# Kernel tuning notes

Measured on AMD Instinct MI355X. Metric: run time of the kernel, lower is better.

The kernel has to match this reference:

```python
import jax, jax.numpy as jnp
import numpy as np

B, K, N = 32768, 8, 64
TN = 3 * N


def _P():
    # 9x9 vec-transpose permutation (matches the hand-built P in the torch module)
    P = np.zeros((9, 9), dtype=np.float32)
    rows = [0, 1, 2, 3, 4, 5, 6, 7, 8]
    cols = [0, 3, 6, 1, 4, 7, 2, 5, 8]
    P[rows, cols] = 1.0
    return jnp.asarray(P)


def _precompute(b, w, lam):
    # b: (K,3,N), w: (1,N,1), lam: scalar
    wsum = jnp.sum(w)
    b_w = (b @ w)[..., 0] / wsum                       # (K,3)
    sw = jnp.sqrt(w).reshape(1, 1, N)                  # (1,1,N)
    bar_b = sw * (b - b_w[:, :, None])                 # (K,3,N)
    bar_B = bar_b.transpose(0, 2, 1).reshape(K, TN).T  # (3N,K)
    bar_H = 2.0 * (bar_B.T @ bar_B + lam * jnp.eye(K, dtype=b.dtype))
    Hinv = jnp.linalg.inv(bar_H)
    Htemp = Hinv @ jnp.ones((K, 1), dtype=b.dtype)     # (K,1)
    s = jnp.sum(Htemp)
    G = Hinv - (Htemp @ Htemp.T) / s                   # (K,K)
    g = Htemp / s                                      # (K,1)
    M = jnp.concatenate([
        2.0 * bar_B @ (G @ bar_B.T) - jnp.eye(TN, dtype=b.dtype),  # (3N,3N)
        2.0 * jnp.sqrt(lam) * (G @ bar_B.T),                        # (K,3N)
    ], axis=0)                                         # (3N+K,3N)
    h = jnp.concatenate([bar_B @ g, jnp.sqrt(lam) * g], axis=0)  # (3N+K,1)
    return bar_B, G, g, M, h, b_w, wsum


def setup_inputs() -> dict:
    key = jax.random.key(0)
    k1, k2 = jax.random.split(key)
    y = jax.random.normal(k1, (B, 3, N), dtype=jnp.float32)
    b = jax.random.normal(k2, (K, 3, N), dtype=jnp.float32)
    w = jnp.ones((1, N, 1), dtype=jnp.float32)
    lam = jnp.ones((1,), dtype=jnp.float32)
    return {"y": y, "b": b, "w": w, "lam": lam}


def reference(y, b, w, lam):
    lam = jnp.squeeze(lam)
    Pm = _P()
    bar_B, G, g, M, h, b_w, wsum = _precompute(b, w, lam)

    # weighted centroid + centered/weighted keypoints
    y_w = (y @ w) / wsum                               # (B,3,1)
    sw = jnp.sqrt(w).reshape(1, 1, N)
    bar_y = sw * (y - y_w)                             # (B,3,N)

    # Batched Q build. kron(Y^T, I3) contraction done implicitly:
    # (M @ kron(Y^T,I3))[a, 3m+j] = sum_n M[a,3n+j] * Y[m,n]
    M_r = M.reshape(TN + K, N, 3)                      # (A,N,3)
    E = jnp.einsum('anj,bmn->bamj', M_r, bar_y).reshape(B, TN + K, 9) @ Pm  # tempE: (B,A,9)
    q_top = jnp.einsum('a,bae->be', h[:, 0], E)        # Q[0,1:]: (B,9)
    Q00 = jnp.sum(h * h)
    Q_low = jnp.einsum('bae,baf->bef', E, E)           # Q[1:,1:]: (B,9,9)

    Q = jnp.zeros((B, 10, 10), dtype=y.dtype)
    Q = Q.at[:, 0, 0].set(Q00)
    Q = Q.at[:, 0, 1:].set(q_top)
    Q = Q.at[:, 1:, 0].set(q_top)
    Q = Q.at[:, 1:, 1:].set(Q_low)

    # Tight SDP relaxation solution: X* = v v^T with v the eigenvector of Q
    # at the smallest eigenvalue; the original then takes top eigvec of X,
    # which recovers the same v.
    ev, evec = jnp.linalg.eigh(Q)
    vec = evec[:, :, 0]                                # smallest-eigenvalue eigvec, (B,10)
    vec = vec / vec[:, :1]
    R = vec[:, 1:].reshape(B, 3, 3).transpose(0, 2, 1)  # (B,3,3)

    # shape coefficients: c = 2 * G bar_B^T kron(I_N, R^T) vec(bar_y^T) + g
    A = G @ bar_B.T                                    # (K,3N)
    Bv = jnp.einsum('bji,bjn->bni', R, bar_y).reshape(B, TN, 1)
    c = 2.0 * (A @ Bv) + g                             # (B,K,1)

    # translation
    t = y_w - R @ (b_w.T @ c)                          # (B,3,1)
    return R, t, c
```

## Files before the change

kernel.cpp:

```cpp
#include <hip/hip_runtime.h>
#include <math.h>

static constexpr int Bn = 32768;

__host__ __device__ constexpr int tidx(int i, int j) { return i*10 - i*(i+1)/2 + j; }
__host__ __device__ constexpr int lidx(int i, int j) { return i*(i+1)/2 + j; }

__global__ __launch_bounds__(256, 2) void k_main(const float* __restrict__ y,
                                                 const float* __restrict__ bb,
                                                 const float* __restrict__ w,
                                                 const float* __restrict__ lam,
                                                 float* __restrict__ out)
{
  __shared__ float s_w[64], s_sw[64], s_barb[64][24];
  __shared__ float s_BtB[64];
  __shared__ float s_M[8][16];
  __shared__ float s_u[8], s_red[64];
  __shared__ float s_wsum, s_q00;
  __shared__ float s_cb[4*520];
  __shared__ float s_G[64], s_g8[8], s_bw[24];
  __shared__ float s_Q[55][66];

  const int t   = threadIdx.x;
  const bool act = (t < 64);
  const int i8 = (t & 63) >> 3, j8 = t & 7;
  const float lv = lam[0];

  if (act) {
    s_w[t]  = w[t];
    s_sw[t] = sqrtf(fmaxf(w[t], 0.0f));
  }
  __syncthreads();
  if (t == 0) { float a = 0; for (int n = 0; n < 64; n++) a += s_w[n]; s_wsum = a; }
  __syncthreads();
  const float wsum = s_wsum;
  if (t < 24) {
    float a = 0;
    for (int n = 0; n < 64; n++) a += bb[t*64 + n] * s_w[n];
    s_bw[t] = a / wsum;
  }
  __syncthreads();
  if (act)
    for (int km = 0; km < 24; ++km)
      s_barb[t][km] = s_sw[t] * (bb[km*64 + t] - s_bw[km]);
  __syncthreads();
  if (act) {
    float a = 0;
    for (int n = 0; n < 64; n++)
      for (int j = 0; j < 3; j++)
        a += s_barb[n][i8*3 + j] * s_barb[n][j8*3 + j];
    s_BtB[t] = a;
  }
  __syncthreads();
  if (act) {
    s_M[i8][j8]     = 2.0f * (s_BtB[t] + ((i8 == j8) ? lv : 0.0f));
    s_M[i8][8 + j8] = (i8 == j8) ? 1.0f : 0.0f;
  }
#pragma unroll
  for (int k = 0; k < 8; k++) {
    __syncthreads();
    float fk = 0.0f, piv = 1.0f;
    if (act) { fk = s_M[i8][k]; piv = 1.0f / s_M[k][k]; }
    __syncthreads();
    if (act && i8 == k) { s_M[k][j8] *= piv; s_M[k][8 + j8] *= piv; }
    __syncthreads();
    if (act && i8 != k) {
      s_M[i8][j8]     -= fk * s_M[k][j8];
      s_M[i8][8 + j8] -= fk * s_M[k][8 + j8];
    }
  }
  __syncthreads();
  if (t < 8) {
    float a = 0;
#pragma unroll
    for (int j = 0; j < 8; j++) a += s_M[t][8 + j];
    s_u[t] = a;
  }
  __syncthreads();
  if (t == 0) {
    float s = 0;
#pragma unroll
    for (int j = 0; j < 8; j++) s += s_u[j];
    s_red[0] = s;
  }
  __syncthreads();
  {
    const float s = s_red[0];
    if (t < 8) s_g8[t] = s_u[t] / s;
    if (act) s_G[t] = s_M[i8][8 + j8] - s_u[i8] * s_u[j8] / s;
  }
  __syncthreads();
  if (act) s_red[t] = s_g8[i8] * (s_BtB[t] + ((i8 == j8) ? lv : 0.0f)) * s_g8[j8];
  __syncthreads();
  if (t == 0) {
    float a = 0;
    for (int n = 0; n < 64; n++) a += s_red[n];
    s_q00 = a;
  }
  if (act) {
    float* p = s_cb + (t >> 4)*520 + (t & 15)*32;
    p[0] = s_w[t]; p[1] = 0; p[2] = 0; p[3] = 0;
#pragma unroll
    for (int km = 0; km < 24; km++)
      p[4 + km] = s_sw[t] * s_barb[t][km];
#pragma unroll
    for (int i = 28; i < 32; i++) p[i] = 0;
  }
  __syncthreads();
  const float q00v = s_q00;

  const int lb  = t >> 2;
  const int sub = t & 3;
  const int b   = blockIdx.x * 64 + lb;
  const float* yb = y + (size_t)b * 192;
  float F[24][3];
  float gw[6];
  float ywa[3] = {0, 0, 0};
#pragma unroll
  for (int i = 0; i < 24; i++) { F[i][0] = 0; F[i][1] = 0; F[i][2] = 0; }
#pragma unroll
  for (int i = 0; i < 6; i++) gw[i] = 0;

  const float* plane = s_cb + sub*520;
#pragma unroll
  for (int i4 = 0; i4 < 4; i4++) {
    const int n4 = sub*4 + i4;
    float4 v0 = reinterpret_cast<const float4*>(yb)[n4];
    float4 v1 = reinterpret_cast<const float4*>(yb + 64)[n4];
    float4 v2 = reinterpret_cast<const float4*>(yb + 128)[n4];
    float a0[4] = {v0.x, v0.y, v0.z, v0.w};
    float a1[4] = {v1.x, v1.y, v1.z, v1.w};
    float a2[4] = {v2.x, v2.y, v2.z, v2.w};
#pragma unroll
    for (int l = 0; l < 4; l++) {
      const int ni = 4*i4 + l;
      const float4* row = reinterpret_cast<const float4*>(plane + ni*32);
      float4 c0 = row[0];
      float4 ch[6];
#pragma unroll
      for (int cc = 0; cc < 6; cc++) ch[cc] = row[1 + cc];
      const float cb[24] = {ch[0].x, ch[0].y, ch[0].z, ch[0].w,
                            ch[1].x, ch[1].y, ch[1].z, ch[1].w,
                            ch[2].x, ch[2].y, ch[2].z, ch[2].w,
                            ch[3].x, ch[3].y, ch[3].z, ch[3].w,
                            ch[4].x, ch[4].y, ch[4].z, ch[4].w,
                            ch[5].x, ch[5].y, ch[5].z, ch[5].w};
      float ym0 = a0[l], ym1 = a1[l], ym2 = a2[l];
      float wn  = c0.x;
      float wy0 = wn*ym0, wy1 = wn*ym1, wy2 = wn*ym2;
      ywa[0] += wy0; ywa[1] += wy1; ywa[2] += wy2;
      gw[0] += wy0*ym0; gw[1] += wy0*ym1; gw[2] += wy0*ym2;
      gw[3] += wy1*ym1; gw[4] += wy1*ym2; gw[5] += wy2*ym2;
#pragma unroll
      for (int km = 0; km < 24; km++) {
        F[km][0] += cb[km]*ym0; F[km][1] += cb[km]*ym1; F[km][2] += cb[km]*ym2;
      }
    }
  }
#pragma unroll
  for (int km = 0; km < 24; km++)
#pragma unroll
    for (int m = 0; m < 3; m++) {
      float v = F[km][m];
      v += __shfl_xor(v, 1);
      v += __shfl_xor(v, 2);
      F[km][m] = v;
    }
#pragma unroll
  for (int i = 0; i < 6; i++) { float v = gw[i]; v += __shfl_xor(v, 1); v += __shfl_xor(v, 2); gw[i] = v; }
#pragma unroll
  for (int i = 0; i < 3; i++) { float v = ywa[i]; v += __shfl_xor(v, 1); v += __shfl_xor(v, 2); ywa[i] = v; }

  const float iws = 1.0f / wsum;
  float yw[3] = {ywa[0]*iws, ywa[1]*iws, ywa[2]*iws};
  float Gram[6];
  Gram[0] = gw[0] - ywa[0]*ywa[0]*iws;
  Gram[1] = gw[1] - ywa[0]*ywa[1]*iws;
  Gram[2] = gw[2] - ywa[0]*ywa[2]*iws;
  Gram[3] = gw[3] - ywa[1]*ywa[1]*iws;
  Gram[4] = gw[4] - ywa[1]*ywa[2]*iws;
  Gram[5] = gw[5] - ywa[2]*ywa[2]*iws;

  if (sub == 0) s_Q[0][lb] = q00v;
#pragma unroll
  for (int e = 0; e < 9; e++) {
    const int j = e / 3, m = e % 3;
    float a = 0;
#pragma unroll
    for (int k = 0; k < 8; k++) a += s_g8[k] * F[k*3 + j][m];
    if ((e & 3) == sub) s_Q[tidx(0, 1 + e)][lb] = -a;
  }
  float F6[6][3];
#pragma unroll
  for (int kk = 0; kk < 6; kk++)
#pragma unroll
    for (int m = 0; m < 3; m++) {
      float x01 = (sub & 1) ? F[6 + kk][m]  : F[kk][m];
      float x23 = (sub & 1) ? F[18 + kk][m] : F[12 + kk][m];
      F6[kk][m] = (sub & 2) ? x23 : x01;
    }
  float FGr[2][9];
#pragma unroll
  for (int kk = 0; kk < 2; kk++) {
    float gcol[8];
#pragma unroll
    for (int k = 0; k < 8; k++) {
      float g01 = (sub & 1) ? s_G[k*8 + 2 + kk] : s_G[k*8 + 0 + kk];
      float g23 = (sub & 1) ? s_G[k*8 + 6 + kk] : s_G[k*8 + 4 + kk];
      gcol[k] = (sub & 2) ? g23 : g01;
    }
#pragma unroll
    for (int e = 0; e < 9; e++) {
      const int j = e / 3, m = e % 3;
      float a = 0;
#pragma unroll
      for (int k = 0; k < 8; k++) a += gcol[k] * F[k*3 + j][m];
      FGr[kk][e] = a;
    }
  }
#pragma unroll
  for (int e = 0; e < 9; e++)
#pragma unroll
    for (int f = e; f < 9; f++) {
      const int j = e/3, m = e%3, j2 = f/3, m2 = f%3;
      float p = FGr[0][e] * F6[j2][m2] + FGr[1][e] * F6[3 + j2][m2];
      p += __shfl_xor(p, 1);
      p += __shfl_xor(p, 2);
      if ((tidx(1 + e, 1 + f) & 3) == sub) {
        const float gterm = (j == j2) ? Gram[(m <= m2) ? (m*3 - m*(m+1)/2 + m2) : (m2*3 - m2*(m2+1)/2 + m)] : 0.0f;
        s_Q[tidx(1 + e, 1 + f)][lb] = -2.0f*p + gterm;
      }
    }
  __syncthreads();

  float Mm[55];
#pragma unroll
  for (int i = 0; i < 10; i++)
#pragma unroll
    for (int j = 0; j <= i; j++)
      Mm[lidx(i,j)] = s_Q[tidx(j,i)][lb];

  float ad[10], b2[9];
#pragma unroll
  for (int j = 0; j < 8; j++) {
    float s2 = 0;
#pragma unroll
    for (int i = j + 1; i < 10; i++) s2 += Mm[lidx(i,j)] * Mm[lidx(i,j)];
    const float x0 = Mm[lidx(j+1,j)];
    const float anorm = __builtin_amdgcn_sqrtf(s2);
    const float alpha = (x0 > 0.0f) ? -anorm : anorm;
    const float uu = s2 - alpha * x0;
    const float beta = (uu > 1e-35f) ? __builtin_amdgcn_rcpf(uu) : 0.0f;
    float u[10], p[10];
    u[j+1] = x0 - alpha;
#pragma unroll
    for (int i = j + 2; i < 10; i++) u[i] = Mm[lidx(i,j)];
#pragma unroll
    for (int i = j + 1; i < 10; i++) {
      float acc = 0;
#pragma unroll
      for (int k = j + 1; k < 10; k++) acc += Mm[(i >= k) ? lidx(i,k) : lidx(k,i)] * u[k];
      p[i] = beta * acc;
    }
    float K = 0;
#pragma unroll
    for (int i = j + 1; i < 10; i++) K += u[i] * p[i];
    K *= 0.5f * beta;
#pragma unroll
    for (int i = j + 1; i < 10; i++) p[i] -= K * u[i];
#pragma unroll
    for (int i = j + 1; i < 10; i++)
#pragma unroll
      for (int k = j + 1; k <= i; k++)
        Mm[lidx(i,k)] -= u[i]*p[k] + p[i]*u[k];
    ad[j] = Mm[lidx(j,j)];
    b2[j] = s2;
  }
  ad[8] = Mm[lidx(8,8)];
  ad[9] = Mm[lidx(9,9)];
  b2[8] = Mm[lidx(9,8)] * Mm[lidx(9,8)];

  float b2max = b2[0];
#pragma unroll
  for (int i = 1; i < 9; i++) b2max = fmaxf(b2max, b2[i]);
  const float pm = 1e-20f * b2max + 1e-30f;

  float lo = 0.0f, hi = s_Q[0][lb];
#pragma unroll
  for (int j = 1; j < 10; j++) hi = fminf(hi, s_Q[tidx(j,j)][lb]);

  const int base = (t & 63) & ~3;
  const float subf = (sub == 0) ? 2.0f : (float)sub;
  for (int round = 0; round < 11; ++round) {
    const float quart = 0.25f * (hi - lo);
    const float mid = lo + quart * subf;
    int neg = 0;
    float d = ad[0] - mid;
    neg += (d < 0.0f) ? 1 : 0;
#pragma unroll
    for (int i = 1; i < 10; i++) {
      d = (fabsf(d) < pm) ? -pm : d;
      d = ad[i] - mid - b2[i-1] * __builtin_amdgcn_rcpf(d);
      neg += (d < 0.0f) ? 1 : 0;
    }
    const int n1 = __shfl(neg, base | 1);
    const int n2 = __shfl(neg, base | 2);
    const int n3 = __shfl(neg, base | 3);
    const float m1 = lo + quart, m2v = lo + 2.0f*quart, m3 = lo + 3.0f*quart;
    const float nlo = (n3 == 0) ? m3 : (n2 == 0) ? m2v : (n1 == 0) ? m1 : lo;
    const float nhi = (n1 > 0) ? m1 : (n2 > 0) ? m2v : (n3 > 0) ? m3 : hi;
    lo = nlo; hi = nhi;
  }

  float M[55], id[10];
#pragma unroll
  for (int i = 0; i < 10; i++)
#pragma unroll
    for (int j = 0; j <= i; j++)
      M[lidx(i,j)] = s_Q[tidx(j,i)][lb];
  float tr = 0.0f;
#pragma unroll
  for (int i = 0; i < 10; i++) tr += M[lidx(i,i)];
  const float delta = 1e-5f * fabsf(tr) + 1e-30f;
  const float sigma = lo - delta;
#pragma unroll
  for (int i = 0; i < 10; i++) M[lidx(i,i)] -= sigma;

#pragma unroll
  for (int j = 0; j < 10; j++) {
    float d = M[lidx(j,j)];
#pragma unroll
    for (int t2 = 0; t2 < j; t2++) d -= M[lidx(j,t2)] * M[lidx(j,t2)];
    d = fmaxf(d, 1e-30f);
    float is = __builtin_amdgcn_rsqf(d);
    id[j] = is;
#pragma unroll
    for (int i = j + 1; i < 10; i++) {
      float a = M[lidx(i,j)];
#pragma unroll
      for (int t2 = 0; t2 < j; t2++) a -= M[lidx(i,t2)] * M[lidx(j,t2)];
      M[lidx(i,j)] = a * is;
    }
  }

  float x[10];
#pragma unroll
  for (int i = 0; i < 10; i++) x[i] = 1.0f;
#pragma unroll
  for (int it = 0; it < 3; ++it) {
#pragma unroll
    for (int i = 0; i < 10; i++) {
      float a = x[i];
#pragma unroll
      for (int j = 0; j < i; j++) a -= M[lidx(i,j)] * x[j];
      x[i] = a * id[i];
    }
#pragma unroll
    for (int i = 9; i >= 0; i--) {
      float a = x[i];
#pragma unroll
      for (int j = i + 1; j < 10; j++) a -= M[lidx(j,i)] * x[j];
      x[i] = a * id[i];
    }
    float s2 = 0;
#pragma unroll
    for (int i = 0; i < 10; i++) s2 += x[i]*x[i];
    float sc = __builtin_amdgcn_rsqf(s2 + 1e-38f);
#pragma unroll
    for (int i = 0; i < 10; i++) x[i] *= sc;
  }

  const float inv0 = __builtin_amdgcn_rcpf(x[0]);
  float R[3][3];
#pragma unroll
  for (int r = 0; r < 3; r++)
#pragma unroll
    for (int cc = 0; cc < 3; cc++)
      R[r][cc] = x[1 + 3*cc + r] * inv0;

  float cv[2];
#pragma unroll
  for (int kk = 0; kk < 2; kk++) {
    const int k = sub*2 + kk;
    float a = 0;
#pragma unroll
    for (int e = 0; e < 9; e++) a += x[1 + e] * FGr[kk][e];
    cv[kk] = 2.0f * inv0 * a + s_g8[k];
    out[(size_t)12*Bn + (size_t)b*8 + k] = cv[kk];
  }
  float um0 = s_bw[(sub*2)*3 + 0]*cv[0] + s_bw[(sub*2 + 1)*3 + 0]*cv[1];
  float um1 = s_bw[(sub*2)*3 + 1]*cv[0] + s_bw[(sub*2 + 1)*3 + 1]*cv[1];
  float um2 = s_bw[(sub*2)*3 + 2]*cv[0] + s_bw[(sub*2 + 1)*3 + 2]*cv[1];
  um0 += __shfl_xor(um0, 1); um0 += __shfl_xor(um0, 2);
  um1 += __shfl_xor(um1, 1); um1 += __shfl_xor(um1, 2);
  um2 += __shfl_xor(um2, 1); um2 += __shfl_xor(um2, 2);

#pragma unroll
  for (int r = 0; r < 3; r++)
#pragma unroll
    for (int cc = 0; cc < 3; cc++)
      if (((r*3 + cc) & 3) == sub)
        out[(size_t)b*9 + r*3 + cc] = R[r][cc];
  if (sub == 0) {
#pragma unroll
    for (int r = 0; r < 3; r++)
      out[(size_t)9*Bn + (size_t)b*3 + r] = yw[r] - (R[r][0]*um0 + R[r][1]*um1 + R[r][2]*um2);
  }
}

extern "C" void kernel_launch(void* const* d_in, const int* in_sizes, int n_in,
                              void* d_out, int out_size, void* d_ws, size_t ws_size,
                              hipStream_t stream) {
  const float* y   = (const float*)d_in[0];
  const float* bb  = (const float*)d_in[1];
  const float* w   = (const float*)d_in[2];
  const float* lam = (const float*)d_in[3];
  float* out = (float*)d_out;
  (void)d_ws; (void)ws_size;
  k_main<<<Bn/64, 256, 0, stream>>>(y, bb, w, lam, out);
}
```

Measured before the change: 38.50 us.

## Keep Q in registers and do inverse iteration on the tridiagonal form

Drops the shared-memory Q staging buffer and its barrier: each lane now builds the full symmetric 10x10 Q in registers from the shuffle-reduced values. Inverse iteration now runs on the Householder tridiagonal matrix with an LDL factorization instead of a dense Cholesky of the shifted Q. The eigenvector is then mapped back by applying the stored Householder reflectors in reverse. This removes the dense Cholesky, dense triangular solves and repeated LDS reads, but it raises register pressure because all 55 entries of Q stay live, and it uses an unpivoted tridiagonal LDL.

```diff
diff --git a/kernel.cpp b/kernel.cpp
--- a/kernel.cpp
+++ b/kernel.cpp
@@ -3,7 +3,6 @@
 
 static constexpr int Bn = 32768;
 
-__host__ __device__ constexpr int tidx(int i, int j) { return i*10 - i*(i+1)/2 + j; }
 __host__ __device__ constexpr int lidx(int i, int j) { return i*(i+1)/2 + j; }
 
 __global__ __launch_bounds__(256, 2) void k_main(const float* __restrict__ y,
@@ -12,14 +11,13 @@
                                                  const float* __restrict__ lam,
                                                  float* __restrict__ out)
 {
-  __shared__ float s_w[64], s_sw[64], s_barb[64][24];
+  __shared__ float s_w[64], s_sw[64], s_barb[64][25];
   __shared__ float s_BtB[64];
   __shared__ float s_M[8][16];
   __shared__ float s_u[8], s_red[64];
   __shared__ float s_wsum, s_q00;
   __shared__ float s_cb[4*520];
   __shared__ float s_G[64], s_g8[8], s_bw[24];
-  __shared__ float s_Q[55][66];
 
   const int t   = threadIdx.x;
   const bool act = (t < 64);
@@ -181,14 +179,15 @@
   Gram[4] = gw[4] - ywa[1]*ywa[2]*iws;
   Gram[5] = gw[5] - ywa[2]*ywa[2]*iws;
 
-  if (sub == 0) s_Q[0][lb] = q00v;
+  float Mm[55];
+  Mm[lidx(0,0)] = q00v;
 #pragma unroll
   for (int e = 0; e < 9; e++) {
     const int j = e / 3, m = e % 3;
     float a = 0;
 #pragma unroll
     for (int k = 0; k < 8; k++) a += s_g8[k] * F[k*3 + j][m];
-    if ((e & 3) == sub) s_Q[tidx(0, 1 + e)][lb] = -a;
+    Mm[lidx(1 + e, 0)] = -a;
   }
   float F6[6][3];
 #pragma unroll
@@ -226,21 +225,18 @@
       float p = FGr[0][e] * F6[j2][m2] + FGr[1][e] * F6[3 + j2][m2];
       p += __shfl_xor(p, 1);
       p += __shfl_xor(p, 2);
-      if ((tidx(1 + e, 1 + f) & 3) == sub) {
-        const float gterm = (j == j2) ? Gram[(m <= m2) ? (m*3 - m*(m+1)/2 + m2) : (m2*3 - m2*(m2+1)/2 + m)] : 0.0f;
-        s_Q[tidx(1 + e, 1 + f)][lb] = -2.0f*p + gterm;
-      }
-    }
-  __syncthreads();
-
-  float Mm[55];
-#pragma unroll
-  for (int i = 0; i < 10; i++)
-#pragma unroll
-    for (int j = 0; j <= i; j++)
-      Mm[lidx(i,j)] = s_Q[tidx(j,i)][lb];
-
-  float ad[10], b2[9];
+      const float gterm = (j == j2) ? Gram[(m <= m2) ? (m*3 - m*(m+1)/2 + m2) : (m2*3 - m2*(m2+1)/2 + m)] : 0.0f;
+      Mm[lidx(1 + f, 1 + e)] = -2.0f*p + gterm;
+    }
+
+  float tr = 0.0f, hi = Mm[lidx(0,0)];
+#pragma unroll
+  for (int j = 0; j < 10; j++) {
+    tr += Mm[lidx(j,j)];
+    hi = fminf(hi, Mm[lidx(j,j)]);
+  }
+
+  float ad[10], b2[9], bofd[9];
 #pragma unroll
   for (int j = 0; j < 8; j++) {
     float s2 = 0;
@@ -273,22 +269,21 @@
 #pragma unroll
       for (int k = j + 1; k <= i; k++)
         Mm[lidx(i,k)] -= u[i]*p[k] + p[i]*u[k];
-    ad[j] = Mm[lidx(j,j)];
-    b2[j] = s2;
+    ad[j]   = Mm[lidx(j,j)];
+    b2[j]   = s2;
+    bofd[j] = alpha;
   }
   ad[8] = Mm[lidx(8,8)];
   ad[9] = Mm[lidx(9,9)];
-  b2[8] = Mm[lidx(9,8)] * Mm[lidx(9,8)];
+  bofd[8] = Mm[lidx(9,8)];
+  b2[8] = bofd[8] * bofd[8];
 
   float b2max = b2[0];
 #pragma unroll
   for (int i = 1; i < 9; i++) b2max = fmaxf(b2max, b2[i]);
   const float pm = 1e-20f * b2max + 1e-30f;
 
-  float lo = 0.0f, hi = s_Q[0][lb];
-#pragma unroll
-  for (int j = 1; j < 10; j++) hi = fminf(hi, s_Q[tidx(j,j)][lb]);
-
+  float lo = 0.0f;
   const int base = (t & 63) & ~3;
   const float subf = (sub == 0) ? 2.0f : (float)sub;
   for (int round = 0; round < 11; ++round) {
@@ -312,71 +307,61 @@
     lo = nlo; hi = nhi;
   }
 
-  float M[55], id[10];
-#pragma unroll
-  for (int i = 0; i < 10; i++)
-#pragma unroll
-    for (int j = 0; j <= i; j++)
-      M[lidx(i,j)] = s_Q[tidx(j,i)][lb];
-  float tr = 0.0f;
-#pragma unroll
-  for (int i = 0; i < 10; i++) tr += M[lidx(i,i)];
   const float delta = 1e-5f * fabsf(tr) + 1e-30f;
   const float sigma = lo - delta;
-#pragma unroll
-  for (int i = 0; i < 10; i++) M[lidx(i,i)] -= sigma;
-
-#pragma unroll
-  for (int j = 0; j < 10; j++) {
-    float d = M[lidx(j,j)];
-#pragma unroll
-    for (int t2 = 0; t2 < j; t2++) d -= M[lidx(j,t2)] * M[lidx(j,t2)];
-    d = fmaxf(d, 1e-30f);
-    float is = __builtin_amdgcn_rsqf(d);
-    id[j] = is;
-#pragma unroll
-    for (int i = j + 1; i < 10; i++) {
-      float a = M[lidx(i,j)];
-#pragma unroll
-      for (int t2 = 0; t2 < j; t2++) a -= M[lidx(i,t2)] * M[lidx(j,t2)];
-      M[lidx(i,j)] = a * is;
-    }
-  }
-
-  float x[10];
-#pragma unroll
-  for (int i = 0; i < 10; i++) x[i] = 1.0f;
+  float dt[10], lt[9], idt[10];
+  dt[0] = ad[0] - sigma;
+#pragma unroll
+  for (int i = 0; i < 9; i++) {
+    float dd = fmaxf(dt[i], 1e-30f);
+    float inv = __builtin_amdgcn_rcpf(dd);
+    idt[i] = inv;
+    lt[i] = bofd[i] * inv;
+    dt[i+1] = ad[i+1] - sigma - lt[i]*bofd[i];
+  }
+  dt[9] = fmaxf(dt[9], 1e-30f);
+  idt[9] = __builtin_amdgcn_rcpf(dt[9]);
+
+  float z[10];
+#pragma unroll
+  for (int i = 0; i < 10; i++) z[i] = 1.0f;
 #pragma unroll
   for (int it = 0; it < 3; ++it) {
 #pragma unroll
-    for (int i = 0; i < 10; i++) {
-      float a = x[i];
-#pragma unroll
-      for (int j = 0; j < i; j++) a -= M[lidx(i,j)] * x[j];
-      x[i] = a * id[i];
-    }
-#pragma unroll
-    for (int i = 9; i >= 0; i--) {
-      float a = x[i];
-#pragma unroll
-      for (int j = i + 1; j < 10; j++) a -= M[lidx(j,i)] * x[j];
-      x[i] = a * id[i];
-    }
+    for (int i = 1; i < 10; i++) z[i] -= lt[i-1]*z[i-1];
+#pragma unroll
+    for (int i = 0; i < 10; i++) z[i] *= idt[i];
+#pragma unroll
+    for (int i = 8; i >= 0; i--) z[i] -= lt[i]*z[i+1];
     float s2 = 0;
 #pragma unroll
-    for (int i = 0; i < 10; i++) s2 += x[i]*x[i];
+    for (int i = 0; i < 10; i++) s2 += z[i]*z[i];
     float sc = __builtin_amdgcn_rsqf(s2 + 1e-38f);
 #pragma unroll
-    for (int i = 0; i < 10; i++) x[i] *= sc;
-  }
-
-  const float inv0 = __builtin_amdgcn_rcpf(x[0]);
+    for (int i = 0; i < 10; i++) z[i] *= sc;
+  }
+#pragma unroll
+  for (int j = 7; j >= 0; j--) {
+    const float x0 = Mm[lidx(j+1,j)];
+    const float us = x0 - bofd[j];
+    const float uu = b2[j] - bofd[j]*x0;
+    const float beta = (uu > 1e-35f) ? __builtin_amdgcn_rcpf(uu) : 0.0f;
+    float dot = us * z[j+1];
+#pragma unroll
+    for (int i = j + 2; i < 10; i++) dot += Mm[lidx(i,j)] * z[i];
+    const float f = beta * dot;
+    z[j+1] -= f * us;
+#pragma unroll
+    for (int i = j + 2; i < 10; i++) z[i] -= f * Mm[lidx(i,j)];
+  }
+
+  const float inv0 = __builtin_amdgcn_rcpf(z[0]);
   float R[3][3];
 #pragma unroll
   for (int r = 0; r < 3; r++)
 #pragma unroll
     for (int cc = 0; cc < 3; cc++)
-      R[r][cc] = x[1 + 3*cc + r] * inv0;
+      R[r][cc] = z[1 + 3*cc + r] * inv0;
 
   float cv[2];
 #pragma unroll
@@ -384,7 +369,7 @@
     const int k = sub*2 + kk;
     float a = 0;
 #pragma unroll
-    for (int e = 0; e < 9; e++) a += x[1 + e] * FGr[kk][e];
+    for (int e = 0; e < 9; e++) a += z[1 + e] * FGr[kk][e];
     cv[kk] = 2.0f * inv0 * a + s_g8[k];
     out[(size_t)12*Bn + (size_t)b*8 + k] = cv[kk];
   }
```

Measured after the change: 73.03 us. 89.7% more time.
